# Kernel tuning notes

Measured on AMD Instinct MI355X. Metric: run time of the kernel, lower is better.

The kernel has to match this reference:

```python
import jax, jax.numpy as jnp
import numpy as np

SELF_OBS_DIM = 18
NEIGHBOR_OBS_DIM = 6
HIDDEN = 256
NUM_NEIGHBORS = 6
BATCH = 131072


def setup_inputs() -> dict:
    key = jax.random.key(0)
    k1, k2, k3, k4, k5, k6 = jax.random.split(key, 6)
    obs_dim = SELF_OBS_DIM + NEIGHBOR_OBS_DIM * NUM_NEIGHBORS
    self_obs = jax.random.normal(k1, (BATCH, SELF_OBS_DIM), dtype=jnp.float32)
    obs = jax.random.normal(k2, (BATCH, obs_dim), dtype=jnp.float32)
    # MLP params (PyTorch Linear default init scale ~ 1/sqrt(fan_in))
    W1 = jax.random.uniform(k3, (NEIGHBOR_OBS_DIM, HIDDEN), minval=-1.0, maxval=1.0) / np.sqrt(NEIGHBOR_OBS_DIM)
    b1 = jax.random.uniform(k4, (HIDDEN,), minval=-1.0, maxval=1.0) / np.sqrt(NEIGHBOR_OBS_DIM)
    W2 = jax.random.uniform(k5, (HIDDEN, HIDDEN), minval=-1.0, maxval=1.0) / np.sqrt(HIDDEN)
    b2 = jax.random.uniform(k6, (HIDDEN,), minval=-1.0, maxval=1.0) / np.sqrt(HIDDEN)
    return {
        "self_obs": self_obs,
        "obs": obs,
        "W1": W1.astype(jnp.float32),
        "b1": b1.astype(jnp.float32),
        "W2": W2.astype(jnp.float32),
        "b2": b2.astype(jnp.float32),
        "all_neighbor_obs_size": NEIGHBOR_OBS_DIM * NUM_NEIGHBORS,
        "batch_size": BATCH,
    }


def reference(self_obs, obs, W1, b1, W2, b2, all_neighbor_obs_size, batch_size):
    # slice out neighbor observations: obs[:, self_obs_dim : self_obs_dim + all_neighbor_obs_size]
    obs_neighbors = obs[:, SELF_OBS_DIM:SELF_OBS_DIM + all_neighbor_obs_size]
    # reshape to per-neighbor rows: [B * num_neighbors, neighbor_obs_dim]
    x = obs_neighbors.reshape(-1, NEIGHBOR_OBS_DIM)
    # shared 2-layer MLP with tanh (sample-factory default nonlinearity)
    h = jnp.tanh(x @ W1 + b1)
    h = jnp.tanh(h @ W2 + b2)
    # [B, num_neighbors, hidden] -> mean over neighbor axis
    neighbor_embeds = h.reshape(batch_size, -1, HIDDEN)
    mean_embed = jnp.mean(neighbor_embeds, axis=1)
    return mean_embed
```

## Files before the change

kernel.cpp:

```cpp
#include <hip/hip_runtime.h>


#define HID     256
#define OBSD    54
#define SELFD   18
#define TILE_B  8
#define TILE_R  48
#define LDA     264
#define LDH     54
#define BATCHN  131072
#define NTILES  (BATCHN / TILE_B)
#define GRID_WG 2048
#define TANH_K  2.8853900817779268f

typedef __attribute__((ext_vector_type(8))) short bf16x8;
typedef __attribute__((ext_vector_type(4))) float f32x4;

__device__ __forceinline__ unsigned cvt_pk_bf16(float lo, float hi) {
    unsigned r;
    asm("v_cvt_pk_bf16_f32 %0, %1, %2" : "=v"(r) : "v"(lo), "v"(hi));
    return r;
}

__device__ __forceinline__ float tanh_fused(float x, float bK) {
    float t = __builtin_amdgcn_exp2f(__builtin_fmaf(x, TANH_K, bK));
    return 1.0f - 2.0f * __builtin_amdgcn_rcpf(t + 1.0f);
}

__device__ __forceinline__ unsigned bfbits(float f) {
    unsigned u = __float_as_uint(f);
    u += 0x7fffu + ((u >> 16) & 1u);
    return u >> 16;
}

__global__ void prep(const float* __restrict__ W1, const float* __restrict__ W2,
                     short* __restrict__ w1t, short* __restrict__ w2t) {
    int idx = blockIdx.x * 256 + threadIdx.x;
    if (idx < 65536) {
        int n = idx >> 8, k = idx & 255;
        w2t[idx] = (short)bfbits(W2[k * HID + n]);
    } else {
        int j = idx - 65536;
        int n = j >> 5, k = j & 31;
        w1t[j] = (k < 6) ? (short)bfbits(W1[k * HID + n]) : (short)0;
    }
}

__global__ __launch_bounds__(256, 2) void qenc_main(
        const float* __restrict__ obs,
        const short* __restrict__ w1t,
        const float* __restrict__ b1,
        const short* __restrict__ w2t,
        const float* __restrict__ b2,
        float* __restrict__ out)
{
    __shared__ union {
        short a[TILE_R * LDA];
        short ht[HID * LDH];
    } u;

    const int tid  = threadIdx.x;
    const int wave = tid >> 6;
    const int lane = tid & 63;
    const int q    = lane >> 4;
    const int c16  = lane & 15;
    const int colbase = wave * 64;

    bf16x8 Bf[8][4];
    #pragma unroll
    for (int kk = 0; kk < 8; ++kk)
        #pragma unroll
        for (int ct = 0; ct < 4; ++ct)
            Bf[kk][ct] = *(const bf16x8*)
                (w2t + (colbase + ct * 16 + c16) * HID + kk * 32 + q * 8);

    float b1s[4][4];
    #pragma unroll
    for (int ct = 0; ct < 4; ++ct)
        #pragma unroll
        for (int g = 0; g < 4; ++g)
            b1s[ct][g] = b1[colbase + ct * 16 + q * 4 + g] * TANH_K;
    float b2s[4];
    #pragma unroll
    for (int ct = 0; ct < 4; ++ct)
        b2s[ct] = b2[colbase + ct * 16 + c16] * TANH_K;

    int soff[3];
    #pragma unroll
    for (int rt = 0; rt < 3; ++rt) {
        int row = rt * 16 + c16;
        soff[rt] = (row / 6) * OBSD + SELFD + (row % 6) * 6;
    }

    for (int tile = blockIdx.x; tile < NTILES; tile += GRID_WG) {
        const size_t obase = (size_t)tile * (TILE_B * OBSD);

        bf16x8 B1f[4];
        #pragma unroll
        for (int ct = 0; ct < 4; ++ct)
            B1f[ct] = *(const bf16x8*)(w1t + (colbase + ct * 16 + c16) * 32 + q * 8);

        #pragma unroll
        for (int rt = 0; rt < 3; ++rt) {
            const float* src = obs + obase + soff[rt];
            float2 f0 = *(const float2*)(src);
            float2 f1 = *(const float2*)(src + 2);
            float2 f2 = *(const float2*)(src + 4);
            union { unsigned w[4]; bf16x8 v; } xf;
            xf.w[0] = cvt_pk_bf16(f0.x, f0.y);
            xf.w[1] = cvt_pk_bf16(f1.x, f1.y);
            xf.w[2] = cvt_pk_bf16(f2.x, f2.y);
            xf.w[3] = 0u;
            #pragma unroll
            for (int ct = 0; ct < 4; ++ct) {
                f32x4 c = __builtin_amdgcn_mfma_f32_16x16x32_bf16(
                    B1f[ct], xf.v, (f32x4){0.f, 0.f, 0.f, 0.f}, 0, 0, 0);
                float t0 = tanh_fused(c[0], b1s[ct][0]);
                float t1 = tanh_fused(c[1], b1s[ct][1]);
                float t2 = tanh_fused(c[2], b1s[ct][2]);
                float t3 = tanh_fused(c[3], b1s[ct][3]);
                uint2 dd;
                dd.x = cvt_pk_bf16(t0, t1);
                dd.y = cvt_pk_bf16(t2, t3);
                *(uint2*)&u.a[(rt * 16 + c16) * LDA + colbase + ct * 16 + q * 4] = dd;
            }
        }
        __syncthreads();

        f32x4 acc[3][4];
        #pragma unroll
        for (int rt = 0; rt < 3; ++rt)
            #pragma unroll
            for (int ct = 0; ct < 4; ++ct) acc[rt][ct] = (f32x4){0.f, 0.f, 0.f, 0.f};

        #pragma unroll
        for (int kk = 0; kk < 8; ++kk) {
            bf16x8 Af[3];
            #pragma unroll
            for (int rt = 0; rt < 3; ++rt)
                Af[rt] = *(const bf16x8*)&u.a[(rt * 16 + c16) * LDA + kk * 32 + q * 8];
            #pragma unroll
            for (int rt = 0; rt < 3; ++rt)
                #pragma unroll
                for (int ct = 0; ct < 4; ++ct)
                    acc[rt][ct] = __builtin_amdgcn_mfma_f32_16x16x32_bf16(
                        Af[rt], Bf[kk][ct], acc[rt][ct], 0, 0, 0);
        }
        __syncthreads();

        #pragma unroll
        for (int ct = 0; ct < 4; ++ct) {
            const int col = colbase + ct * 16 + c16;
            #pragma unroll
            for (int rt = 0; rt < 3; ++rt) {
                float t0 = tanh_fused(acc[rt][ct][0], b2s[ct]);
                float t1 = tanh_fused(acc[rt][ct][1], b2s[ct]);
                float t2 = tanh_fused(acc[rt][ct][2], b2s[ct]);
                float t3 = tanh_fused(acc[rt][ct][3], b2s[ct]);
                const int row = rt * 16 + q * 4;
                *(unsigned*)&u.ht[col * LDH + row]     = cvt_pk_bf16(t0, t1);
                *(unsigned*)&u.ht[col * LDH + row + 2] = cvt_pk_bf16(t2, t3);
            }
        }

        const int b0 = tile * TILE_B;
        #pragma unroll
        for (int bl = 0; bl < TILE_B; ++bl) {
            const unsigned* p = (const unsigned*)&u.ht[tid * LDH + bl * 6];
            float s = 0.f;
            #pragma unroll
            for (int d = 0; d < 3; ++d) {
                unsigned uu = p[d];
                s += __uint_as_float(uu << 16) + __uint_as_float(uu & 0xffff0000u);
            }
            out[(size_t)(b0 + bl) * HID + tid] = s * (1.0f / 6.0f);
        }
        __syncthreads();
    }
}

extern "C" void kernel_launch(void* const* d_in, const int* in_sizes, int n_in,
                              void* d_out, int out_size, void* d_ws, size_t ws_size,
                              hipStream_t stream) {
    const float* obs = (const float*)d_in[1];
    const float* W1  = (const float*)d_in[2];
    const float* b1  = (const float*)d_in[3];
    const float* W2  = (const float*)d_in[4];
    const float* b2  = (const float*)d_in[5];
    float* outp = (float*)d_out;

    short* w2t = (short*)d_ws;
    short* w1t = (short*)((char*)d_ws + 131072);

    prep<<<288, 256, 0, stream>>>(W1, W2, w1t, w2t);
    qenc_main<<<GRID_WG, 256, 0, stream>>>(obs, w1t, b1, w2t, b2, outp);
}
```

Baseline: 344.8 us.

## Split hidden columns across 16 waves with 1024-thread workgroups

Workgroups grow from 4 to 16 waves, and each wave now owns 16 hidden columns instead of 64. Per-wave register use for the W2 fragments and accumulators drops about fourfold, which should allow more waves resident per CU and better latency hiding. The W1 fragment load is hoisted out of the tile loop, and the final mean/store is redistributed so each lane handles two batch rows for its column. The cost is that the same 48-row A tile is now read from LDS by more waves, and barriers must synchronise 16 waves instead of 4.

```diff
diff --git a/kernel.cpp b/kernel.cpp
--- a/kernel.cpp
+++ b/kernel.cpp
@@ -46,7 +46,7 @@
     }
 }
 
-__global__ __launch_bounds__(256, 2) void qenc_main(
+__global__ __launch_bounds__(1024, 4) void qenc_main(
         const float* __restrict__ obs,
         const short* __restrict__ w1t,
         const float* __restrict__ b1,
@@ -64,26 +64,20 @@
     const int lane = tid & 63;
     const int q    = lane >> 4;
     const int c16  = lane & 15;
-    const int colbase = wave * 64;
+    const int colbase = wave * 16;
 
-    bf16x8 Bf[8][4];
+    bf16x8 Bf[8];
     #pragma unroll
     for (int kk = 0; kk < 8; ++kk)
-        #pragma unroll
-        for (int ct = 0; ct < 4; ++ct)
-            Bf[kk][ct] = *(const bf16x8*)
-                (w2t + (colbase + ct * 16 + c16) * HID + kk * 32 + q * 8);
+        Bf[kk] = *(const bf16x8*)(w2t + (colbase + c16) * HID + kk * 32 + q * 8);
 
-    float b1s[4][4];
+    bf16x8 B1f = *(const bf16x8*)(w1t + (colbase + c16) * 32 + q * 8);
+
+    float b1s[4];
     #pragma unroll
-    for (int ct = 0; ct < 4; ++ct)
-        #pragma unroll
-        for (int g = 0; g < 4; ++g)
-            b1s[ct][g] = b1[colbase + ct * 16 + q * 4 + g] * TANH_K;
-    float b2s[4];
-    #pragma unroll
-    for (int ct = 0; ct < 4; ++ct)
-        b2s[ct] = b2[colbase + ct * 16 + c16] * TANH_K;
+    for (int g = 0; g < 4; ++g)
+        b1s[g] = b1[colbase + q * 4 + g] * TANH_K;
+    const float b2s = b2[colbase + c16] * TANH_K;
 
     int soff[3];
     #pragma unroll
@@ -94,11 +88,6 @@
 
     for (int tile = blockIdx.x; tile < NTILES; tile += GRID_WG) {
         const size_t obase = (size_t)tile * (TILE_B * OBSD);
-
-        bf16x8 B1f[4];
-        #pragma unroll
-        for (int ct = 0; ct < 4; ++ct)
-            B1f[ct] = *(const bf16x8*)(w1t + (colbase + ct * 16 + c16) * 32 + q * 8);
 
         #pragma unroll
         for (int rt = 0; rt < 3; ++rt) {
@@ -111,27 +100,22 @@
             xf.w[1] = cvt_pk_bf16(f1.x, f1.y);
             xf.w[2] = cvt_pk_bf16(f2.x, f2.y);
             xf.w[3] = 0u;
-            #pragma unroll
-            for (int ct = 0; ct < 4; ++ct) {
-                f32x4 c = __builtin_amdgcn_mfma_f32_16x16x32_bf16(
-                    B1f[ct], xf.v, (f32x4){0.f, 0.f, 0.f, 0.f}, 0, 0, 0);
-                float t0 = tanh_fused(c[0], b1s[ct][0]);
-                float t1 = tanh_fused(c[1], b1s[ct][1]);
-                float t2 = tanh_fused(c[2], b1s[ct][2]);
-                float t3 = tanh_fused(c[3], b1s[ct][3]);
-                uint2 dd;
-                dd.x = cvt_pk_bf16(t0, t1);
-                dd.y = cvt_pk_bf16(t2, t3);
-                *(uint2*)&u.a[(rt * 16 + c16) * LDA + colbase + ct * 16 + q * 4] = dd;
-            }
+            f32x4 c = __builtin_amdgcn_mfma_f32_16x16x32_bf16(
+                B1f, xf.v, (f32x4){0.f, 0.f, 0.f, 0.f}, 0, 0, 0);
+            float t0 = tanh_fused(c[0], b1s[0]);
+            float t1 = tanh_fused(c[1], b1s[1]);
+            float t2 = tanh_fused(c[2], b1s[2]);
+            float t3 = tanh_fused(c[3], b1s[3]);
+            uint2 dd;
+            dd.x = cvt_pk_bf16(t0, t1);
+            dd.y = cvt_pk_bf16(t2, t3);
+            *(uint2*)&u.a[(rt * 16 + c16) * LDA + colbase + q * 4] = dd;
         }
         __syncthreads();
 
-        f32x4 acc[3][4];
+        f32x4 acc[3];
         #pragma unroll
-        for (int rt = 0; rt < 3; ++rt)
-            #pragma unroll
-            for (int ct = 0; ct < 4; ++ct) acc[rt][ct] = (f32x4){0.f, 0.f, 0.f, 0.f};
+        for (int rt = 0; rt < 3; ++rt) acc[rt] = (f32x4){0.f, 0.f, 0.f, 0.f};
 
         #pragma unroll
         for (int kk = 0; kk < 8; ++kk) {
@@ -141,22 +125,19 @@
                 Af[rt] = *(const bf16x8*)&u.a[(rt * 16 + c16) * LDA + kk * 32 + q * 8];
             #pragma unroll
             for (int rt = 0; rt < 3; ++rt)
-                #pragma unroll
-                for (int ct = 0; ct < 4; ++ct)
-                    acc[rt][ct] = __builtin_amdgcn_mfma_f32_16x16x32_bf16(
-                        Af[rt], Bf[kk][ct], acc[rt][ct], 0, 0, 0);
+                acc[rt] = __builtin_amdgcn_mfma_f32_16x16x32_bf16(
+                    Af[rt], Bf[kk], acc[rt], 0, 0, 0);
         }
         __syncthreads();
 
-        #pragma unroll
-        for (int ct = 0; ct < 4; ++ct) {
-            const int col = colbase + ct * 16 + c16;
+        {
+            const int col = colbase + c16;
             #pragma unroll
             for (int rt = 0; rt < 3; ++rt) {
-                float t0 = tanh_fused(acc[rt][ct][0], b2s[ct]);
-                float t1 = tanh_fused(acc[rt][ct][1], b2s[ct]);
-                float t2 = tanh_fused(acc[rt][ct][2], b2s[ct]);
-                float t3 = tanh_fused(acc[rt][ct][3], b2s[ct]);
+                float t0 = tanh_fused(acc[rt][0], b2s);
+                float t1 = tanh_fused(acc[rt][1], b2s);
+                float t2 = tanh_fused(acc[rt][2], b2s);
+                float t3 = tanh_fused(acc[rt][3], b2s);
                 const int row = rt * 16 + q * 4;
                 *(unsigned*)&u.ht[col * LDH + row]     = cvt_pk_bf16(t0, t1);
                 *(unsigned*)&u.ht[col * LDH + row + 2] = cvt_pk_bf16(t2, t3);
@@ -164,16 +145,20 @@
         }
 
         const int b0 = tile * TILE_B;
-        #pragma unroll
-        for (int bl = 0; bl < TILE_B; ++bl) {
-            const unsigned* p = (const unsigned*)&u.ht[tid * LDH + bl * 6];
-            float s = 0.f;
+        {
+            const int col = colbase + c16;
             #pragma unroll
-            for (int d = 0; d < 3; ++d) {
-                unsigned uu = p[d];
-                s += __uint_as_float(uu << 16) + __uint_as_float(uu & 0xffff0000u);
+            for (int jj = 0; jj < 2; ++jj) {
+                const int bl = q * 2 + jj;
+                const unsigned* p = (const unsigned*)&u.ht[col * LDH + bl * 6];
+                float s = 0.f;
+                #pragma unroll
+                for (int d = 0; d < 3; ++d) {
+                    unsigned uu = p[d];
+                    s += __uint_as_float(uu << 16) + __uint_as_float(uu & 0xffff0000u);
+                }
+                out[(size_t)(b0 + bl) * HID + col] = s * (1.0f / 6.0f);
             }
-            out[(size_t)(b0 + bl) * HID + tid] = s * (1.0f / 6.0f);
         }
         __syncthreads();
     }
@@ -193,5 +178,5 @@
     short* w1t = (short*)((char*)d_ws + 131072);
 
     prep<<<288, 256, 0, stream>>>(W1, W2, w1t, w2t);
-    qenc_main<<<GRID_WG, 256, 0, stream>>>(obs, w1t, b1, w2t, b2, outp);
+    qenc_main<<<GRID_WG, 1024, 0, stream>>>(obs, w1t, b1, w2t, b2, outp);
 }
```

After: 455.5 us. 1.32x slower.
